# Kernel optimization log

Hardware: AMD Instinct MI355X
Metric: run time of the kernel (lower is better)

The kernel has to match this reference:

```python
import jax, jax.numpy as jnp
import numpy as np
import math

N_HEAD = 16

def setup_inputs() -> dict:
    key = jax.random.key(0)
    k1, k2, k3 = jax.random.split(key, 3)
    B, T, C = 4, 2048, 1024
    x = jax.random.normal(k1, (B, T, C), dtype=jnp.float32)
    W_attn = jax.random.normal(k2, (C, 3 * C), dtype=jnp.float32) * 0.02
    b_attn = jnp.zeros((3 * C,), dtype=jnp.float32)
    W_proj = jax.random.normal(k3, (C, C), dtype=jnp.float32) * 0.02
    b_proj = jnp.zeros((C,), dtype=jnp.float32)
    return {"x": x, "W_attn": W_attn, "b_attn": b_attn, "W_proj": W_proj, "b_proj": b_proj}

def reference(x, W_attn, b_attn, W_proj, b_proj):
    B, T, C = x.shape
    H = N_HEAD
    hd = C // H
    qkv = x @ W_attn + b_attn                      # [B,T,3C]
    # Faithful to source bug: q, k, v ALL built from the k-slice of qkv.
    k_slice = qkv[:, :, C:2 * C]
    k = k_slice.reshape(B, T, H, hd).transpose(0, 2, 1, 3)  # [B,H,T,hd]
    q = k
    v = k
    att = jnp.einsum('bhqd,bhkd->bhqk', q, k) / math.sqrt(hd)  # [B,H,T,T]
    causal = jnp.tril(jnp.ones((T, T), dtype=bool))
    att = jnp.where(causal[None, None], att, jnp.finfo(att.dtype).min)
    att = jax.nn.softmax(att, axis=-1)
    y = jnp.einsum('bhqk,bhkd->bhqd', att, v)      # [B,H,T,hd]
    y = y.transpose(0, 2, 1, 3).reshape(B, T, C)
    return y @ W_proj + b_proj
```

## Files before the change

### kernel.cpp

```cpp
#include <hip/hip_runtime.h>

#define T_SEQ 2048
#define C_DIM 1024
#define HD 64

typedef __attribute__((ext_vector_type(8))) short short8;
typedef __attribute__((ext_vector_type(4))) float f32x4;
typedef __attribute__((ext_vector_type(4))) unsigned int uint4v;

extern "C" __device__ float __ocml_native_exp2_f32(float);

__device__ __forceinline__ unsigned short f2bf(float f) {
  unsigned int u = __builtin_bit_cast(unsigned int, f);
  u += 0x7fffu + ((u >> 16) & 1u);
  return (unsigned short)(u >> 16);
}

__device__ __forceinline__ unsigned cvt_pk_bf16(float lo, float hi) {
  unsigned r;
  asm("v_cvt_pk_bf16_f32 %0, %1, %2" : "=v"(r) : "v"(lo), "v"(hi));
  return r;
}

__device__ __forceinline__ void gload_lds16(const void* g, void* l) {
  __builtin_amdgcn_global_load_lds(
      (const __attribute__((address_space(1))) void*)g,
      (__attribute__((address_space(3))) void*)l, 16, 0, 0);
}

__global__ __launch_bounds__(256) void transpose_w(
    const float* __restrict__ src, unsigned short* __restrict__ dst,
    int src_ld, int col_off) {
  int n = blockIdx.x * 16 + threadIdx.x;
  int k = blockIdx.y * 16 + threadIdx.y;
  dst[(size_t)n * C_DIM + k] = f2bf(src[(size_t)k * src_ld + col_off + n]);
}

__global__ __launch_bounds__(256) void gemm_xw(
    const float* __restrict__ A, const unsigned short* __restrict__ Bt,
    const float* __restrict__ bias, unsigned short* __restrict__ out,
    unsigned short* __restrict__ vt) {
  __shared__ unsigned short Als[128][40];
  __shared__ unsigned short Bls[128 * 32];
  const int tid = threadIdx.x;
  const int l = tid & 63, w = tid >> 6;
  const int wr = w >> 1, wc = w & 1;
  const int rb = blockIdx.x * 128, cb = blockIdx.y * 128;
  const int srow = tid >> 1, sh = (tid & 1) * 16;
  const int brow = tid >> 2, bhalf = (tid & 3) * 8;
  f32x4 acc[4][4] = {};
  for (int kb = 0; kb < 1024; kb += 32) {
    gload_lds16(Bt + (size_t)(cb + brow) * 1024 + kb + bhalf,
                &Bls[(size_t)w * 512]);
    gload_lds16(Bt + (size_t)(cb + 64 + brow) * 1024 + kb + bhalf,
                &Bls[2048 + (size_t)w * 512]);
    const f32x4* ap = (const f32x4*)(A + (size_t)(rb + srow) * 1024 + kb + sh);
    f32x4 a0 = ap[0], a1 = ap[1], a2 = ap[2], a3 = ap[3];
    short8 s0, s1;
#pragma unroll
    for (int i = 0; i < 4; ++i) {
      s0[i]     = (short)f2bf(a0[i]);
      s0[i + 4] = (short)f2bf(a1[i]);
      s1[i]     = (short)f2bf(a2[i]);
      s1[i + 4] = (short)f2bf(a3[i]);
    }
    *(short8*)&Als[srow][sh] = s0;
    *(short8*)&Als[srow][sh + 8] = s1;
    __syncthreads();
    short8 af[4], bfr[4];
#pragma unroll
    for (int m = 0; m < 4; ++m)
      af[m] = *(const short8*)&Als[wr * 64 + m * 16 + (l & 15)][(l >> 4) * 8];
#pragma unroll
    for (int n = 0; n < 4; ++n)
      bfr[n] = *(const short8*)&Bls[(wc * 64 + n * 16 + (l & 15)) * 32 + (l >> 4) * 8];
#pragma unroll
    for (int m = 0; m < 4; ++m)
#pragma unroll
      for (int n = 0; n < 4; ++n)
        acc[m][n] = __builtin_amdgcn_mfma_f32_16x16x32_bf16(af[m], bfr[n], acc[m][n], 0, 0, 0);
    __syncthreads();
  }
  const int rg = (l >> 4) * 4, cg = l & 15;
#pragma unroll
  for (int m = 0; m < 4; ++m)
#pragma unroll
    for (int n = 0; n < 4; ++n) {
      int col = cb + wc * 64 + n * 16 + cg;
      float bv = bias[col];
      int row0 = rb + wr * 64 + m * 16 + rg;
      unsigned short e0 = f2bf(acc[m][n][0] + bv);
      unsigned short e1 = f2bf(acc[m][n][1] + bv);
      unsigned short e2 = f2bf(acc[m][n][2] + bv);
      unsigned short e3 = f2bf(acc[m][n][3] + bv);
      size_t bhd = (size_t)((row0 >> 11) * 16 + (col >> 6));
      size_t kidx = (bhd * T_SEQ + (row0 & 2047)) * HD + (col & 63);
      out[kidx]          = e0;
      out[kidx + HD]     = e1;
      out[kidx + 2 * HD] = e2;
      out[kidx + 3 * HD] = e3;
      unsigned long long pv = (unsigned long long)e0 | ((unsigned long long)e1 << 16)
                            | ((unsigned long long)e2 << 32) | ((unsigned long long)e3 << 48);
      *(unsigned long long*)&vt[(bhd * HD + (col & 63)) * T_SEQ + (row0 & 2047)] = pv;
    }
}

__global__ __launch_bounds__(256) void gemm_yw(
    const unsigned short* __restrict__ A, const unsigned short* __restrict__ Bt,
    const float* __restrict__ bias, float* __restrict__ out) {
  __shared__ unsigned short Als[128 * 32];
  __shared__ unsigned short Bls[128 * 32];
  const int tid = threadIdx.x;
  const int l = tid & 63, w = tid >> 6;
  const int wr = w >> 1, wc = w & 1;
  const int rb = blockIdx.x * 128, cb = blockIdx.y * 128;
  const int brow = tid >> 2, bhalf = (tid & 3) * 8;
  f32x4 acc[4][4] = {};
  for (int kb = 0; kb < 1024; kb += 32) {
    gload_lds16(A + (size_t)(rb + brow) * 1024 + kb + bhalf,
                &Als[(size_t)w * 512]);
    gload_lds16(A + (size_t)(rb + 64 + brow) * 1024 + kb + bhalf,
                &Als[2048 + (size_t)w * 512]);
    gload_lds16(Bt + (size_t)(cb + brow) * 1024 + kb + bhalf,
                &Bls[(size_t)w * 512]);
    gload_lds16(Bt + (size_t)(cb + 64 + brow) * 1024 + kb + bhalf,
                &Bls[2048 + (size_t)w * 512]);
    __syncthreads();
    short8 af[4], bfr[4];
#pragma unroll
    for (int m = 0; m < 4; ++m)
      af[m] = *(const short8*)&Als[(wr * 64 + m * 16 + (l & 15)) * 32 + (l >> 4) * 8];
#pragma unroll
    for (int n = 0; n < 4; ++n)
      bfr[n] = *(const short8*)&Bls[(wc * 64 + n * 16 + (l & 15)) * 32 + (l >> 4) * 8];
#pragma unroll
    for (int m = 0; m < 4; ++m)
#pragma unroll
      for (int n = 0; n < 4; ++n)
        acc[m][n] = __builtin_amdgcn_mfma_f32_16x16x32_bf16(af[m], bfr[n], acc[m][n], 0, 0, 0);
    __syncthreads();
  }
  const int rg = (l >> 4) * 4, cg = l & 15;
#pragma unroll
  for (int m = 0; m < 4; ++m)
#pragma unroll
    for (int n = 0; n < 4; ++n) {
      int col = cb + wc * 64 + n * 16 + cg;
      float bv = bias[col];
#pragma unroll
      for (int r = 0; r < 4; ++r) {
        int row = rb + wr * 64 + m * 16 + rg + r;
        out[(size_t)row * 1024 + col] = acc[m][n][r] + bv;
      }
    }
}

__device__ __forceinline__ void sm_group(
    f32x4 (&s)[4], int qq, int kvb, bool needmask, int g,
    float& mrun, float& lrun, f32x4 (&yacc)[4],
    int src01, int src23, bool hi2, short8 (&pa)[2]) {
  if (needmask) {
    const int lim = qq - kvb;
#pragma unroll
    for (int b = 0; b < 4; ++b)
#pragma unroll
      for (int r = 0; r < 4; ++r)
        if (16 * b + 4 * g + r > lim) s[b][r] = -INFINITY;
  }
  float mt = fmaxf(fmaxf(s[0][0], s[0][1]), fmaxf(s[0][2], s[0][3]));
#pragma unroll
  for (int b = 1; b < 4; ++b)
    mt = fmaxf(mt, fmaxf(fmaxf(s[b][0], s[b][1]), fmaxf(s[b][2], s[b][3])));
  mt = fmaxf(mt, __shfl_xor(mt, 16));
  mt = fmaxf(mt, __shfl_xor(mt, 32));
  if (!__all(mt <= mrun + 11.5416f)) {
    float mn = fmaxf(mrun, mt);
    float al = __ocml_native_exp2_f32(mrun - mn);
    mrun = mn;
    lrun *= al;
    float a0 = __shfl(al, 4 * g + 0);
    float a1 = __shfl(al, 4 * g + 1);
    float a2 = __shfl(al, 4 * g + 2);
    float a3 = __shfl(al, 4 * g + 3);
#pragma unroll
    for (int nb = 0; nb < 4; ++nb) {
      yacc[nb][0] *= a0; yacc[nb][1] *= a1;
      yacc[nb][2] *= a2; yacc[nb][3] *= a3;
    }
  }
  float ps = 0.f;
  unsigned pk[4][2];
#pragma unroll
  for (int b = 0; b < 4; ++b) {
    float p0 = __ocml_native_exp2_f32(s[b][0] - mrun);
    float p1 = __ocml_native_exp2_f32(s[b][1] - mrun);
    float p2 = __ocml_native_exp2_f32(s[b][2] - mrun);
    float p3 = __ocml_native_exp2_f32(s[b][3] - mrun);
    ps += (p0 + p1) + (p2 + p3);
    pk[b][0] = cvt_pk_bf16(p0, p1);
    pk[b][1] = cvt_pk_bf16(p2, p3);
  }
  ps += __shfl_xor(ps, 16);
  ps += __shfl_xor(ps, 32);
  lrun += ps;
  {
    unsigned x0a = (unsigned)__shfl((int)pk[0][0], src01);
    unsigned x1a = (unsigned)__shfl((int)pk[1][0], src01);
    unsigned x0b = (unsigned)__shfl((int)pk[0][1], src01);
    unsigned x1b = (unsigned)__shfl((int)pk[1][1], src01);
    unsigned y0a = (unsigned)__shfl((int)pk[0][0], src23);
    unsigned y1a = (unsigned)__shfl((int)pk[1][0], src23);
    unsigned y0b = (unsigned)__shfl((int)pk[0][1], src23);
    unsigned y1b = (unsigned)__shfl((int)pk[1][1], src23);
    uint4v u;
    u.x = hi2 ? x1a : x0a;
    u.y = hi2 ? x1b : x0b;
    u.z = hi2 ? y1a : y0a;
    u.w = hi2 ? y1b : y0b;
    pa[0] = __builtin_bit_cast(short8, u);
  }
  {
    unsigned x0a = (unsigned)__shfl((int)pk[2][0], src01);
    unsigned x1a = (unsigned)__shfl((int)pk[3][0], src01);
    unsigned x0b = (unsigned)__shfl((int)pk[2][1], src01);
    unsigned x1b = (unsigned)__shfl((int)pk[3][1], src01);
    unsigned y0a = (unsigned)__shfl((int)pk[2][0], src23);
    unsigned y1a = (unsigned)__shfl((int)pk[3][0], src23);
    unsigned y0b = (unsigned)__shfl((int)pk[2][1], src23);
    unsigned y1b = (unsigned)__shfl((int)pk[3][1], src23);
    uint4v u;
    u.x = hi2 ? x1a : x0a;
    u.y = hi2 ? x1b : x0b;
    u.z = hi2 ? y1a : y0a;
    u.w = hi2 ? y1b : y0b;
    pa[1] = __builtin_bit_cast(short8, u);
  }
}

__global__ __launch_bounds__(128, 4) void attn_fwd(
    const unsigned short* __restrict__ Khb, const unsigned short* __restrict__ Vt,
    unsigned short* __restrict__ Y) {
  const int id = blockIdx.x;
  const int xcd = id & 7;
  const int r8  = id >> 3;
  const int bh  = xcd * 8 + (r8 & 7);
  const int chunk = 63 - (r8 >> 3);
  const int tid = threadIdx.x;
  const int w = tid >> 6;
  const int l = tid & 63;
  const int i = l & 15, g = l >> 4;
  const unsigned short* kbase = Khb + (size_t)bh * T_SEQ * HD;
  const unsigned short* vbase = Vt + (size_t)bh * HD * T_SEQ;

  const int q0 = chunk * 32;
  const int qA = q0 + i, qB = q0 + 16 + i;
  const int nt = (q0 + 31) / 64 + 1;
  const int half = (nt + 1) >> 1;
  const int tBeg = w ? half : 0;
  const int tEnd = w ? nt : half;

  __shared__ float Ylds[32][68];
  __shared__ float Mlds[32];
  __shared__ float Llds[32];

  short8 qa0 = *(const short8*)(kbase + (size_t)qA * HD + g * 8);
  short8 qa1 = *(const short8*)(kbase + (size_t)qA * HD + 32 + g * 8);
  short8 qb0 = *(const short8*)(kbase + (size_t)qB * HD + g * 8);
  short8 qb1 = *(const short8*)(kbase + (size_t)qB * HD + 32 + g * 8);

  f32x4 ya[4] = {}, yb[4] = {};
  float mA = -INFINITY, lA = 0.f, mB = -INFINITY, lB = 0.f;

  const int src01 = i + ((g & 1) << 5);
  const int src23 = src01 + 16;
  const bool hi2 = (g >> 1) != 0;
  const float SCL = 0.18033688f;

  for (int t = tBeg; t < tEnd; ++t) {
    const int kvb = t * 64;
    f32x4 sa[4], sb[4];
#pragma unroll
    for (int b = 0; b < 4; ++b) {
      const unsigned short* kp = kbase + (size_t)(kvb + 16 * b + i) * HD + g * 8;
      short8 k0 = *(const short8*)kp;
      short8 k1 = *(const short8*)(kp + 32);
      f32x4 acc = {};
      acc = __builtin_amdgcn_mfma_f32_16x16x32_bf16(k0, qa0, acc, 0, 0, 0);
      acc = __builtin_amdgcn_mfma_f32_16x16x32_bf16(k1, qa1, acc, 0, 0, 0);
      sa[b] = acc;
      f32x4 acc2 = {};
      acc2 = __builtin_amdgcn_mfma_f32_16x16x32_bf16(k0, qb0, acc2, 0, 0, 0);
      acc2 = __builtin_amdgcn_mfma_f32_16x16x32_bf16(k1, qb1, acc2, 0, 0, 0);
      sb[b] = acc2;
    }
#pragma unroll
    for (int b = 0; b < 4; ++b)
#pragma unroll
      for (int r = 0; r < 4; ++r) { sa[b][r] *= SCL; sb[b][r] *= SCL; }

    const bool needmask = (kvb + 63 > q0);
    short8 paA[2], paB[2];
    sm_group(sa, qA, kvb, needmask, g, mA, lA, ya, src01, src23, hi2, paA);
    sm_group(sb, qB, kvb, needmask, g, mB, lB, yb, src01, src23, hi2, paB);

#pragma unroll
    for (int c = 0; c < 2; ++c)
#pragma unroll
      for (int nb = 0; nb < 4; ++nb) {
        short8 vf = *(const short8*)(vbase + (size_t)(nb * 16 + i) * T_SEQ + kvb + c * 32 + g * 8);
        ya[nb] = __builtin_amdgcn_mfma_f32_16x16x32_bf16(paA[c], vf, ya[nb], 0, 0, 0);
        yb[nb] = __builtin_amdgcn_mfma_f32_16x16x32_bf16(paB[c], vf, yb[nb], 0, 0, 0);
      }
  }

  if (w == 1) {
#pragma unroll
    for (int nb = 0; nb < 4; ++nb)
#pragma unroll
      for (int r = 0; r < 4; ++r) {
        Ylds[4 * g + r][nb * 16 + i]      = ya[nb][r];
        Ylds[16 + 4 * g + r][nb * 16 + i] = yb[nb][r];
      }
    if (l < 16) {
      Mlds[l]      = mA;
      Llds[l]      = lA;
      Mlds[16 + l] = mB;
      Llds[16 + l] = lB;
    }
  }
  __syncthreads();
  if (w == 0) {
    const int bb = bh >> 4, hh = bh & 15;
    size_t rowA = ((size_t)bb * T_SEQ + q0 + 4 * g) * C_DIM;
#pragma unroll
    for (int r = 0; r < 4; ++r) {
      float m0 = __shfl(mA, 4 * g + r);
      float l0 = __shfl(lA, 4 * g + r);
      float m1 = Mlds[4 * g + r];
      float l1 = Llds[4 * g + r];
      float mm = fmaxf(m0, m1);
      float e0 = __ocml_native_exp2_f32(m0 - mm);
      float e1 = __ocml_native_exp2_f32(m1 - mm);
      float inv = 1.f / (l0 * e0 + l1 * e1);
      float w0 = e0 * inv, w1 = e1 * inv;
#pragma unroll
      for (int nb = 0; nb < 4; ++nb) {
        int col = hh * 64 + nb * 16 + i;
        Y[rowA + (size_t)r * C_DIM + col] =
            f2bf(ya[nb][r] * w0 + Ylds[4 * g + r][nb * 16 + i] * w1);
      }
    }
    size_t rowB = rowA + (size_t)16 * C_DIM;
#pragma unroll
    for (int r = 0; r < 4; ++r) {
      float m0 = __shfl(mB, 4 * g + r);
      float l0 = __shfl(lB, 4 * g + r);
      float m1 = Mlds[16 + 4 * g + r];
      float l1 = Llds[16 + 4 * g + r];
      float mm = fmaxf(m0, m1);
      float e0 = __ocml_native_exp2_f32(m0 - mm);
      float e1 = __ocml_native_exp2_f32(m1 - mm);
      float inv = 1.f / (l0 * e0 + l1 * e1);
      float w0 = e0 * inv, w1 = e1 * inv;
#pragma unroll
      for (int nb = 0; nb < 4; ++nb) {
        int col = hh * 64 + nb * 16 + i;
        Y[rowB + (size_t)r * C_DIM + col] =
            f2bf(yb[nb][r] * w0 + Ylds[16 + 4 * g + r][nb * 16 + i] * w1);
      }
    }
  }
}

extern "C" void kernel_launch(void* const* d_in, const int* in_sizes, int n_in,
                              void* d_out, int out_size, void* d_ws, size_t ws_size,
                              hipStream_t stream) {
  const float* x      = (const float*)d_in[0];
  const float* W_attn = (const float*)d_in[1];
  const float* b_attn = (const float*)d_in[2];
  const float* W_proj = (const float*)d_in[3];
  const float* b_proj = (const float*)d_in[4];
  float* out = (float*)d_out;

  unsigned short* Wkt  = (unsigned short*)d_ws;
  unsigned short* Wpt  = Wkt + (size_t)1024 * 1024;
  unsigned short* Khb  = Wpt + (size_t)1024 * 1024;
  unsigned short* Ybuf = Khb + (size_t)8192 * 1024;
  unsigned short* Vtb  = Ybuf + (size_t)8192 * 1024;

  transpose_w<<<dim3(64, 64), dim3(16, 16), 0, stream>>>(W_attn, Wkt, 3072, 1024);
  transpose_w<<<dim3(64, 64), dim3(16, 16), 0, stream>>>(W_proj, Wpt, 1024, 0);

  gemm_xw<<<dim3(64, 8), 256, 0, stream>>>(x, Wkt, b_attn + 1024, Khb, Vtb);

  attn_fwd<<<dim3(4096), 128, 0, stream>>>(Khb, Vtb, Ybuf);

  gemm_yw<<<dim3(64, 8), 256, 0, stream>>>(Ybuf, Wpt, b_proj, out);
}
```

Baseline: 211.0 us.

## Split attention KV range across four waves with tree-reduced softmax merge

The attention kernel now uses 256 threads per block and splits the key/value tiles of each query chunk across four waves instead of two. Partial outputs and softmax statistics are combined in two rounds through shared memory, with extra barriers. The XCD-aware block-to-head mapping is also replaced by a simple modulo mapping. This adds parallelism for the long causal rows, at the cost of more LDS traffic and synchronisation and possibly worse L2 locality per XCD.

Result: slower. 219.9 us (+4.3%).

```diff
diff --git a/kernel.cpp b/kernel.cpp
--- a/kernel.cpp
+++ b/kernel.cpp
@@ -237,14 +237,12 @@
   }
 }
 
-__global__ __launch_bounds__(128, 4) void attn_fwd(
+__global__ __launch_bounds__(256, 4) void attn_fwd(
     const unsigned short* __restrict__ Khb, const unsigned short* __restrict__ Vt,
     unsigned short* __restrict__ Y) {
   const int id = blockIdx.x;
-  const int xcd = id & 7;
-  const int r8  = id >> 3;
-  const int bh  = xcd * 8 + (r8 & 7);
-  const int chunk = 63 - (r8 >> 3);
+  const int bh = id & 63;
+  const int chunk = 63 - (id >> 6);
   const int tid = threadIdx.x;
   const int w = tid >> 6;
   const int l = tid & 63;
@@ -255,13 +253,13 @@
   const int q0 = chunk * 32;
   const int qA = q0 + i, qB = q0 + 16 + i;
   const int nt = (q0 + 31) / 64 + 1;
-  const int half = (nt + 1) >> 1;
-  const int tBeg = w ? half : 0;
-  const int tEnd = w ? nt : half;
-
-  __shared__ float Ylds[32][68];
-  __shared__ float Mlds[32];
-  __shared__ float Llds[32];
+  const int per = (nt + 3) >> 2;
+  const int tBeg = min(w * per, nt);
+  const int tEnd = min(tBeg + per, nt);
+
+  __shared__ float Ylds[2][32][68];
+  __shared__ float Mlds[2][32];
+  __shared__ float Llds[2][32];
 
   short8 qa0 = *(const short8*)(kbase + (size_t)qA * HD + g * 8);
   short8 qa1 = *(const short8*)(kbase + (size_t)qA * HD + 32 + g * 8);
@@ -313,19 +311,72 @@
       }
   }
 
-  if (w == 1) {
+  if (w == 1 || w == 3) {
+    const int s = (w == 1) ? 0 : 1;
 #pragma unroll
     for (int nb = 0; nb < 4; ++nb)
 #pragma unroll
       for (int r = 0; r < 4; ++r) {
-        Ylds[4 * g + r][nb * 16 + i]      = ya[nb][r];
-        Ylds[16 + 4 * g + r][nb * 16 + i] = yb[nb][r];
+        Ylds[s][4 * g + r][nb * 16 + i]      = ya[nb][r];
+        Ylds[s][16 + 4 * g + r][nb * 16 + i] = yb[nb][r];
       }
     if (l < 16) {
-      Mlds[l]      = mA;
-      Llds[l]      = lA;
-      Mlds[16 + l] = mB;
-      Llds[16 + l] = lB;
+      Mlds[s][l]      = mA;
+      Llds[s][l]      = lA;
+      Mlds[s][16 + l] = mB;
+      Llds[s][16 + l] = lB;
+    }
+  }
+  __syncthreads();
+  if (w == 0 || w == 2) {
+    const int s = (w == 0) ? 0 : 1;
+    {
+      float m1 = Mlds[s][i], l1 = Llds[s][i];
+      float mm = fmaxf(mA, m1);
+      float eS = (mA == mm) ? 1.f : __ocml_native_exp2_f32(mA - mm);
+      float eO = (m1 == mm) ? 1.f : __ocml_native_exp2_f32(m1 - mm);
+      lA = lA * eS + l1 * eO;
+      mA = mm;
+#pragma unroll
+      for (int r = 0; r < 4; ++r) {
+        float sS = __shfl(eS, 4 * g + r);
+        float sO = __shfl(eO, 4 * g + r);
+#pragma unroll
+        for (int nb = 0; nb < 4; ++nb)
+          ya[nb][r] = ya[nb][r] * sS + Ylds[s][4 * g + r][nb * 16 + i] * sO;
+      }
+    }
+    {
+      float m1 = Mlds[s][16 + i], l1 = Llds[s][16 + i];
+      float mm = fmaxf(mB, m1);
+      float eS = (mB == mm) ? 1.f : __ocml_native_exp2_f32(mB - mm);
+      float eO = (m1 == mm) ? 1.f : __ocml_native_exp2_f32(m1 - mm);
+      lB = lB * eS + l1 * eO;
+      mB = mm;
+#pragma unroll
+      for (int r = 0; r < 4; ++r) {
+        float sS = __shfl(eS, 4 * g + r);
+        float sO = __shfl(eO, 4 * g + r);
+#pragma unroll
+        for (int nb = 0; nb < 4; ++nb)
+          yb[nb][r] = yb[nb][r] * sS + Ylds[s][16 + 4 * g + r][nb * 16 + i] * sO;
+      }
+    }
+  }
+  __syncthreads();
+  if (w == 2) {
+#pragma unroll
+    for (int nb = 0; nb < 4; ++nb)
+#pragma unroll
+      for (int r = 0; r < 4; ++r) {
+        Ylds[0][4 * g + r][nb * 16 + i]      = ya[nb][r];
+        Ylds[0][16 + 4 * g + r][nb * 16 + i] = yb[nb][r];
+      }
+    if (l < 16) {
+      Mlds[0][l]      = mA;
+      Llds[0][l]      = lA;
+      Mlds[0][16 + l] = mB;
+      Llds[0][16 + l] = lB;
     }
   }
   __syncthreads();
@@ -336,8 +387,8 @@
     for (int r = 0; r < 4; ++r) {
       float m0 = __shfl(mA, 4 * g + r);
       float l0 = __shfl(lA, 4 * g + r);
-      float m1 = Mlds[4 * g + r];
-      float l1 = Llds[4 * g + r];
+      float m1 = Mlds[0][4 * g + r];
+      float l1 = Llds[0][4 * g + r];
       float mm = fmaxf(m0, m1);
       float e0 = __ocml_native_exp2_f32(m0 - mm);
       float e1 = __ocml_native_exp2_f32(m1 - mm);
@@ -347,7 +398,7 @@
       for (int nb = 0; nb < 4; ++nb) {
         int col = hh * 64 + nb * 16 + i;
         Y[rowA + (size_t)r * C_DIM + col] =
-            f2bf(ya[nb][r] * w0 + Ylds[4 * g + r][nb * 16 + i] * w1);
+            f2bf(ya[nb][r] * w0 + Ylds[0][4 * g + r][nb * 16 + i] * w1);
       }
     }
     size_t rowB = rowA + (size_t)16 * C_DIM;
@@ -355,8 +406,8 @@
     for (int r = 0; r < 4; ++r) {
       float m0 = __shfl(mB, 4 * g + r);
       float l0 = __shfl(lB, 4 * g + r);
-      float m1 = Mlds[16 + 4 * g + r];
-      float l1 = Llds[16 + 4 * g + r];
+      float m1 = Mlds[0][16 + 4 * g + r];
+      float l1 = Llds[0][16 + 4 * g + r];
       float mm = fmaxf(m0, m1);
       float e0 = __ocml_native_exp2_f32(m0 - mm);
       float e1 = __ocml_native_exp2_f32(m1 - mm);
@@ -366,7 +417,7 @@
       for (int nb = 0; nb < 4; ++nb) {
         int col = hh * 64 + nb * 16 + i;
         Y[rowB + (size_t)r * C_DIM + col] =
-            f2bf(yb[nb][r] * w0 + Ylds[16 + 4 * g + r][nb * 16 + i] * w1);
+            f2bf(yb[nb][r] * w0 + Ylds[0][16 + 4 * g + r][nb * 16 + i] * w1);
       }
     }
   }
@@ -393,7 +444,7 @@
 
   gemm_xw<<<dim3(64, 8), 256, 0, stream>>>(x, Wkt, b_attn + 1024, Khb, Vtb);
 
-  attn_fwd<<<dim3(4096), 128, 0, stream>>>(Khb, Vtb, Ybuf);
+  attn_fwd<<<dim3(4096), 256, 0, stream>>>(Khb, Vtb, Ybuf);
 
   gemm_yw<<<dim3(64, 8), 256, 0, stream>>>(Ybuf, Wpt, b_proj, out);
 }
```

## Pre-convert x to bf16 and stream A tiles via direct LDS loads; prioritize MFMA

Applied to the files above, without the earlier changes.

Adds a separate pass that converts x from fp32 to bf16 into the Ybuf workspace. The QKV GEMM then loads both operands with global_load_lds instead of converting fp32 to bf16 inside every K iteration, which removes per-block conversion work and halves the A-tile bytes the GEMM reads. The cost is an extra kernel launch plus a full write and reread of x in bf16. The attention loop also raises wave priority with s_setprio around its MFMA sections so that matrix work is issued ahead of the softmax work of other waves.

Measured after the change: 205.7 us. -2.5%, faster.

```diff
diff --git a/kernel.cpp b/kernel.cpp
--- a/kernel.cpp
+++ b/kernel.cpp
@@ -36,41 +36,46 @@
   dst[(size_t)n * C_DIM + k] = f2bf(src[(size_t)k * src_ld + col_off + n]);
 }
 
+__global__ __launch_bounds__(256) void conv_x(
+    const float* __restrict__ x, unsigned short* __restrict__ xb) {
+  size_t idx = ((size_t)blockIdx.x * 256 + threadIdx.x) * 8;
+  const f32x4* p = (const f32x4*)(x + idx);
+  f32x4 a = p[0], b = p[1];
+  short8 s;
+#pragma unroll
+  for (int i = 0; i < 4; ++i) {
+    s[i]     = (short)f2bf(a[i]);
+    s[i + 4] = (short)f2bf(b[i]);
+  }
+  *(short8*)(xb + idx) = s;
+}
+
 __global__ __launch_bounds__(256) void gemm_xw(
-    const float* __restrict__ A, const unsigned short* __restrict__ Bt,
+    const unsigned short* __restrict__ A, const unsigned short* __restrict__ Bt,
     const float* __restrict__ bias, unsigned short* __restrict__ out,
     unsigned short* __restrict__ vt) {
-  __shared__ unsigned short Als[128][40];
+  __shared__ unsigned short Als[128 * 32];
   __shared__ unsigned short Bls[128 * 32];
   const int tid = threadIdx.x;
   const int l = tid & 63, w = tid >> 6;
   const int wr = w >> 1, wc = w & 1;
   const int rb = blockIdx.x * 128, cb = blockIdx.y * 128;
-  const int srow = tid >> 1, sh = (tid & 1) * 16;
   const int brow = tid >> 2, bhalf = (tid & 3) * 8;
   f32x4 acc[4][4] = {};
   for (int kb = 0; kb < 1024; kb += 32) {
+    gload_lds16(A + (size_t)(rb + brow) * 1024 + kb + bhalf,
+                &Als[(size_t)w * 512]);
+    gload_lds16(A + (size_t)(rb + 64 + brow) * 1024 + kb + bhalf,
+                &Als[2048 + (size_t)w * 512]);
     gload_lds16(Bt + (size_t)(cb + brow) * 1024 + kb + bhalf,
                 &Bls[(size_t)w * 512]);
     gload_lds16(Bt + (size_t)(cb + 64 + brow) * 1024 + kb + bhalf,
                 &Bls[2048 + (size_t)w * 512]);
-    const f32x4* ap = (const f32x4*)(A + (size_t)(rb + srow) * 1024 + kb + sh);
-    f32x4 a0 = ap[0], a1 = ap[1], a2 = ap[2], a3 = ap[3];
-    short8 s0, s1;
-#pragma unroll
-    for (int i = 0; i < 4; ++i) {
-      s0[i]     = (short)f2bf(a0[i]);
-      s0[i + 4] = (short)f2bf(a1[i]);
-      s1[i]     = (short)f2bf(a2[i]);
-      s1[i + 4] = (short)f2bf(a3[i]);
-    }
-    *(short8*)&Als[srow][sh] = s0;
-    *(short8*)&Als[srow][sh + 8] = s1;
     __syncthreads();
     short8 af[4], bfr[4];
 #pragma unroll
     for (int m = 0; m < 4; ++m)
-      af[m] = *(const short8*)&Als[wr * 64 + m * 16 + (l & 15)][(l >> 4) * 8];
+      af[m] = *(const short8*)&Als[(wr * 64 + m * 16 + (l & 15)) * 32 + (l >> 4) * 8];
 #pragma unroll
     for (int n = 0; n < 4; ++n)
       bfr[n] = *(const short8*)&Bls[(wc * 64 + n * 16 + (l & 15)) * 32 + (l >> 4) * 8];
@@ -279,6 +284,7 @@
   for (int t = tBeg; t < tEnd; ++t) {
     const int kvb = t * 64;
     f32x4 sa[4], sb[4];
+    __builtin_amdgcn_s_setprio(1);
 #pragma unroll
     for (int b = 0; b < 4; ++b) {
       const unsigned short* kp = kbase + (size_t)(kvb + 16 * b + i) * HD + g * 8;
@@ -293,6 +299,7 @@
       acc2 = __builtin_amdgcn_mfma_f32_16x16x32_bf16(k1, qb1, acc2, 0, 0, 0);
       sb[b] = acc2;
     }
+    __builtin_amdgcn_s_setprio(0);
 #pragma unroll
     for (int b = 0; b < 4; ++b)
 #pragma unroll
@@ -303,6 +310,7 @@
     sm_group(sa, qA, kvb, needmask, g, mA, lA, ya, src01, src23, hi2, paA);
     sm_group(sb, qB, kvb, needmask, g, mB, lB, yb, src01, src23, hi2, paB);
 
+    __builtin_amdgcn_s_setprio(1);
 #pragma unroll
     for (int c = 0; c < 2; ++c)
 #pragma unroll
@@ -311,6 +319,7 @@
         ya[nb] = __builtin_amdgcn_mfma_f32_16x16x32_bf16(paA[c], vf, ya[nb], 0, 0, 0);
         yb[nb] = __builtin_amdgcn_mfma_f32_16x16x32_bf16(paB[c], vf, yb[nb], 0, 0, 0);
       }
+    __builtin_amdgcn_s_setprio(0);
   }
 
   if (w == 1) {
@@ -387,11 +396,14 @@
   unsigned short* Khb  = Wpt + (size_t)1024 * 1024;
   unsigned short* Ybuf = Khb + (size_t)8192 * 1024;
   unsigned short* Vtb  = Ybuf + (size_t)8192 * 1024;
+  unsigned short* xb   = Ybuf;
 
   transpose_w<<<dim3(64, 64), dim3(16, 16), 0, stream>>>(W_attn, Wkt, 3072, 1024);
   transpose_w<<<dim3(64, 64), dim3(16, 16), 0, stream>>>(W_proj, Wpt, 1024, 0);
 
-  gemm_xw<<<dim3(64, 8), 256, 0, stream>>>(x, Wkt, b_attn + 1024, Khb, Vtb);
+  conv_x<<<dim3(4096), 256, 0, stream>>>(x, xb);
+
+  gemm_xw<<<dim3(64, 8), 256, 0, stream>>>(xb, Wkt, b_attn + 1024, Khb, Vtb);
 
   attn_fwd<<<dim3(4096), 128, 0, stream>>>(Khb, Vtb, Ybuf);
 
```
